# Kernel optimization log

Measured on AMD Instinct MI355X. Metric: run time of the kernel, lower is better.

Reference implementation:

```python
import jax, jax.numpy as jnp
import numpy as np
from math import factorial, sqrt

# ---- e3nn-style real Wigner-3j (Clebsch-Gordan) construction ----
L1, L2, LOUT, LMID = 3, 3, 3, 4

def _cg_coef(j1, m1, j2, m2, j3, m3):
    if m1 + m2 != m3:
        return 0.0
    f = factorial
    vmin = max(0, j2 - j3 - m1, j1 - j3 + m2)
    vmax = min(j1 + j2 - j3, j1 - m1, j2 + m2)
    pref = sqrt((2 * j3 + 1) * f(j3 + j1 - j2) * f(j3 - j1 + j2) * f(j1 + j2 - j3) / f(j1 + j2 + j3 + 1))
    pref *= sqrt(f(j3 + m3) * f(j3 - m3) * f(j1 + m1) * f(j1 - m1) * f(j2 + m2) * f(j2 - m2))
    s = 0.0
    for v in range(vmin, vmax + 1):
        s += (-1) ** v / (f(v) * f(j1 + j2 - j3 - v) * f(j1 - m1 - v) * f(j2 + m2 - v)
                          * f(j3 - j2 + m1 + v) * f(j3 - j1 - m2 + v))
    return pref * s

def _su2_cg(l1, l2, l3):
    C = np.zeros((2 * l1 + 1, 2 * l2 + 1, 2 * l3 + 1))
    for m1 in range(-l1, l1 + 1):
        for m2 in range(-l2, l2 + 1):
            m3 = m1 + m2
            if -l3 <= m3 <= l3:
                C[l1 + m1, l2 + m2, l3 + m3] = _cg_coef(l1, m1, l2, m2, l3, m3)
    return C

def _q(l):  # real->complex SH change of basis (e3nn convention)
    q = np.zeros((2 * l + 1, 2 * l + 1), dtype=np.complex128)
    for m in range(-l, 0):
        q[l + m, l + abs(m)] = 1 / np.sqrt(2)
        q[l + m, l - abs(m)] = -1j / np.sqrt(2)
    q[l, l] = 1.0
    for m in range(1, l + 1):
        q[l + m, l + abs(m)] = (-1) ** m / np.sqrt(2)
        q[l + m, l - abs(m)] = 1j * (-1) ** m / np.sqrt(2)
    return (-1j) ** l * q

def _w3j(l1, l2, l3):
    C = _su2_cg(l1, l2, l3).astype(np.complex128)
    C = np.einsum('ij,kl,mn,ikn->jlm', _q(l1), _q(l2), np.conj(_q(l3).T), C)
    C = np.real(C)
    return (C / np.linalg.norm(C)).astype(np.float32)

def _instructions(lmax1, lmax2, lmax_out):
    ins = [(a, b, c)
           for a in range(lmax1 + 1) for b in range(lmax2 + 1) for c in range(lmax_out + 1)
           if abs(a - b) <= c <= a + b and (a + b + c) % 2 == 0]
    cnt = {}
    for _, _, c in ins:
        cnt[c] = cnt.get(c, 0) + 1
    # normalization='component', path_normalization='element' with all mul=1
    pw = np.array([sqrt((2 * c + 1) / cnt[c]) for _, _, c in ins], dtype=np.float32)
    return ins, pw

INS1, PW1 = _instructions(L1, L2, LMID)      # 27 paths
INS21, PW21 = _instructions(L1, LMID, LOUT)  # 27 paths
INS22, PW22 = _instructions(L2, LMID, LOUT)  # 27 paths
W3J = {k: jnp.asarray(_w3j(*k)) for k in set(INS1) | set(INS21) | set(INS22)}

def _tp(x, y, w, ins, pw, lmax_out):
    # FullyConnectedTensorProduct with multiplicity-1 SH irreps.
    # x: [E, (l1+1)^2], y: [E, (l2+1)^2] -> [E, (lmax_out+1)^2]
    out = jnp.zeros((x.shape[0], (lmax_out + 1) ** 2), dtype=x.dtype)
    for i, (a, b, c) in enumerate(ins):
        xa = x[:, a * a:(a + 1) ** 2]
        yb = y[:, b * b:(b + 1) ** 2]
        z = jnp.einsum('ijk,ei,ej->ek', W3J[(a, b, c)], xa, yb)
        out = out.at[:, c * c:(c + 1) ** 2].add((pw[i] * w[i]) * z)
    return out

E, C = 200000, 16
B = (LOUT + 1) ** 2  # 16

def setup_inputs() -> dict:
    k = jax.random.split(jax.random.key(0), 5)
    return {
        'x': jax.random.normal(k[0], (E, B, C), jnp.float32),
        'y': jax.random.normal(k[1], (E, B, C), jnp.float32),
        'w1': jax.random.normal(k[2], (len(INS1),), jnp.float32),
        'w21': jax.random.normal(k[3], (len(INS21),), jnp.float32),
        'w22': jax.random.normal(k[4], (len(INS22),), jnp.float32),
    }

def reference(x, y, w1, w21, w22):
    xm = x.mean(2)  # [E, 16]
    ym = y.mean(2)  # [E, 16]
    mid = _tp(xm, ym, w1, INS1, PW1, LMID)  # [E, 25]
    out = (x + y
           + _tp(xm, mid, w21, INS21, PW21, LOUT)[..., None]
           + _tp(ym, mid, w22, INS22, PW22, LOUT)[..., None])
    return out
```

## Files before the change

kernel.cpp:

```cpp
#include <hip/hip_runtime.h>


struct W3JT { double v[9][9][9]; };

constexpr double dfact(int n) { double r = 1.0; for (int i = 2; i <= n; ++i) r *= (double)i; return r; }

constexpr double csqrt(double x) {
  if (x <= 0.0) return 0.0;
  double g = x > 1.0 ? x : 1.0;
  for (int i = 0; i < 80; ++i) g = 0.5 * (g + x / g);
  return g;
}

constexpr double cg_coef(int j1, int m1, int j2, int m2, int j3, int m3) {
  if (m1 + m2 != m3) return 0.0;
  int vmin = 0;
  if (j2 - j3 - m1 > vmin) vmin = j2 - j3 - m1;
  if (j1 - j3 + m2 > vmin) vmin = j1 - j3 + m2;
  int vmax = j1 + j2 - j3;
  if (j1 - m1 < vmax) vmax = j1 - m1;
  if (j2 + m2 < vmax) vmax = j2 + m2;
  double pref = csqrt((2.0 * j3 + 1.0) * dfact(j3 + j1 - j2) * dfact(j3 - j1 + j2) * dfact(j1 + j2 - j3) / dfact(j1 + j2 + j3 + 1));
  pref *= csqrt(dfact(j3 + m3) * dfact(j3 - m3) * dfact(j1 + m1) * dfact(j1 - m1) * dfact(j2 + m2) * dfact(j2 - m2));
  double s = 0.0;
  for (int v = vmin; v <= vmax; ++v) {
    double t = 1.0 / (dfact(v) * dfact(j1 + j2 - j3 - v) * dfact(j1 - m1 - v) * dfact(j2 + m2 - v) * dfact(j3 - j2 + m1 + v) * dfact(j3 - j1 - m2 + v));
    s += (v & 1) ? -t : t;
  }
  return pref * s;
}

struct QCol { int n; int row[2]; double re[2]; double im[2]; };

constexpr QCol qcol(int l, int col) {
  QCol q{};
  const int lm = l & 3;
  const double pr = (lm == 0) ? 1.0 : (lm == 2) ? -1.0 : 0.0;
  const double pi = (lm == 1) ? -1.0 : (lm == 3) ? 1.0 : 0.0;
  const int mu = col - l;
  const int am = mu < 0 ? -mu : mu;
  const double is2 = 0.70710678118654752440;
  if (mu == 0) {
    q.n = 1; q.row[0] = l;
    q.re[0] = pr; q.im[0] = pi;
  } else {
    const double s = (am & 1) ? -1.0 : 1.0;
    double a0 = 0.0, b0 = 0.0, a1 = 0.0, b1 = 0.0;
    if (mu > 0) { a0 = is2; b0 = 0.0;  a1 = s * is2; b1 = 0.0; }
    else        { a0 = 0.0; b0 = -is2; a1 = 0.0;     b1 = s * is2; }
    q.n = 2;
    q.row[0] = l - am; q.row[1] = l + am;
    q.re[0] = a0 * pr - b0 * pi; q.im[0] = a0 * pi + b0 * pr;
    q.re[1] = a1 * pr - b1 * pi; q.im[1] = a1 * pi + b1 * pr;
  }
  return q;
}

constexpr W3JT make_w3j(int l1, int l2, int l3) {
  W3JT R{};
  double C[9][9][9]{};
  for (int m1 = -l1; m1 <= l1; ++m1)
    for (int m2 = -l2; m2 <= l2; ++m2) {
      int m3 = m1 + m2;
      if (m3 >= -l3 && m3 <= l3)
        C[l1 + m1][l2 + m2][l3 + m3] = cg_coef(l1, m1, l2, m2, l3, m3);
    }
  double nrm = 0.0;
  for (int j = 0; j < 2 * l1 + 1; ++j) {
    QCol q1 = qcol(l1, j);
    for (int l = 0; l < 2 * l2 + 1; ++l) {
      QCol q2 = qcol(l2, l);
      for (int m = 0; m < 2 * l3 + 1; ++m) {
        QCol q3 = qcol(l3, m);
        double re = 0.0;
        for (int a = 0; a < q1.n; ++a)
          for (int b = 0; b < q2.n; ++b)
            for (int c = 0; c < q3.n; ++c) {
              double cv = C[q1.row[a]][q2.row[b]][q3.row[c]];
              if (cv == 0.0) continue;
              double ar = q1.re[a], ai = q1.im[a];
              double br = q2.re[b], bi = q2.im[b];
              double cr = q3.re[c], ci = -q3.im[c];
              double abr = ar * br - ai * bi;
              double abi = ar * bi + ai * br;
              double prr = abr * cr - abi * ci;
              re += prr * cv;
            }
        R.v[j][l][m] = re;
        nrm += re * re;
      }
    }
  }
  double n = csqrt(nrm);
  if (n > 0.0)
    for (int j = 0; j < 2 * l1 + 1; ++j)
      for (int l = 0; l < 2 * l2 + 1; ++l)
        for (int m = 0; m < 2 * l3 + 1; ++m)
          R.v[j][l][m] /= n;
  return R;
}

constexpr int CNT1[5] = {4, 6, 7, 6, 4};
constexpr int CNT2[4] = {4, 7, 8, 8};

#define NZCHK(V) ((V) > 1e-12 || (V) < -1e-12)

#define TP_MID(IDX, A, B, C) do { \
  constexpr W3JT T = make_w3j(A, B, C); \
  constexpr double PW = csqrt((2.0 * (C) + 1.0) / (double)CNT1[(C)]); \
  const float wi = w1p[IDX]; \
  float u[2 * (A) + 1]; \
  _Pragma("unroll") for (int i = 0; i < 2 * (A) + 1; ++i) u[i] = wi * xm[(A) * (A) + i]; \
  _Pragma("unroll") for (int i = 0; i < 2 * (A) + 1; ++i) { \
    _Pragma("unroll") for (int j = 0; j < 2 * (B) + 1; ++j) { \
      const float p_ = u[i] * ym[(B) * (B) + j]; \
      _Pragma("unroll") for (int k = 0; k < 2 * (C) + 1; ++k) { \
        if (NZCHK(T.v[i][j][k])) \
          mid[(C) * (C) + k] = __builtin_fmaf((float)(T.v[i][j][k] * PW), p_, mid[(C) * (C) + k]); \
      } \
    } \
  } \
} while (0)

#define TP_OUT(IDX, A, B, C) do { \
  constexpr W3JT T = make_w3j(A, B, C); \
  constexpr double PW = csqrt((2.0 * (C) + 1.0) / (double)CNT2[(C)]); \
  const float wa = w21p[IDX]; \
  const float wb = w22p[IDX]; \
  float u[2 * (A) + 1]; \
  _Pragma("unroll") for (int i = 0; i < 2 * (A) + 1; ++i) \
    u[i] = wa * xm[(A) * (A) + i] + wb * ym[(A) * (A) + i]; \
  _Pragma("unroll") for (int i = 0; i < 2 * (A) + 1; ++i) { \
    _Pragma("unroll") for (int j = 0; j < 2 * (B) + 1; ++j) { \
      const float p_ = u[i] * mid[(B) * (B) + j]; \
      _Pragma("unroll") for (int k = 0; k < 2 * (C) + 1; ++k) { \
        if (NZCHK(T.v[i][j][k])) \
          tv[(C) * (C) + k] = __builtin_fmaf((float)(T.v[i][j][k] * PW), p_, tv[(C) * (C) + k]); \
      } \
    } \
  } \
} while (0)

typedef float f32x4 __attribute__((ext_vector_type(4)));

__global__ __launch_bounds__(256) void cg2_v3(
    const float4* __restrict__ x4, const float4* __restrict__ y4,
    const float* __restrict__ w1p, const float* __restrict__ w21p,
    const float* __restrict__ w22p, float4* __restrict__ o4, int E)
{
  const int t = blockIdx.x * 256 + threadIdx.x;
  const int e = t >> 2;
  if (e >= E) return;
  const int g = t & 3;
  const int base = e * 64 + g;

  float4 s[16];
  float px[16], py[16];
#pragma unroll
  for (int k = 0; k < 16; ++k) {
    const float4 xv = x4[base + 4 * k];
    const float4 yv = y4[base + 4 * k];
    s[k].x = xv.x + yv.x; s[k].y = xv.y + yv.y;
    s[k].z = xv.z + yv.z; s[k].w = xv.w + yv.w;
    px[k] = (xv.x + xv.y) + (xv.z + xv.w);
    py[k] = (yv.x + yv.y) + (yv.z + yv.w);
  }

  float xm[16], ym[16];
#pragma unroll
  for (int k = 0; k < 16; ++k) {
    float rx = px[k] + __shfl_xor(px[k], 1);
    rx += __shfl_xor(rx, 2);
    float ry = py[k] + __shfl_xor(py[k], 1);
    ry += __shfl_xor(ry, 2);
    xm[k] = rx * (1.0f / 16.0f);
    ym[k] = ry * (1.0f / 16.0f);
  }

  float mid[25];
#pragma unroll
  for (int k = 0; k < 25; ++k) mid[k] = 0.f;

  TP_MID( 0, 0, 0, 0);
  TP_MID( 1, 0, 1, 1);
  TP_MID( 2, 0, 2, 2);
  TP_MID( 3, 0, 3, 3);
  TP_MID( 4, 1, 0, 1);
  TP_MID( 5, 1, 1, 0);
  TP_MID( 6, 1, 1, 2);
  TP_MID( 7, 1, 2, 1);
  TP_MID( 8, 1, 2, 3);
  TP_MID( 9, 1, 3, 2);
  TP_MID(10, 1, 3, 4);
  TP_MID(11, 2, 0, 2);
  TP_MID(12, 2, 1, 1);
  TP_MID(13, 2, 1, 3);
  TP_MID(14, 2, 2, 0);
  TP_MID(15, 2, 2, 2);
  TP_MID(16, 2, 2, 4);
  TP_MID(17, 2, 3, 1);
  TP_MID(18, 2, 3, 3);
  TP_MID(19, 3, 0, 3);
  TP_MID(20, 3, 1, 2);
  TP_MID(21, 3, 1, 4);
  TP_MID(22, 3, 2, 1);
  TP_MID(23, 3, 2, 3);
  TP_MID(24, 3, 3, 0);
  TP_MID(25, 3, 3, 2);
  TP_MID(26, 3, 3, 4);

  float tv[16];
#pragma unroll
  for (int k = 0; k < 16; ++k) tv[k] = 0.f;

  TP_OUT( 0, 0, 0, 0);
  TP_OUT( 1, 0, 1, 1);
  TP_OUT( 2, 0, 2, 2);
  TP_OUT( 3, 0, 3, 3);
  TP_OUT( 4, 1, 0, 1);
  TP_OUT( 5, 1, 1, 0);
  TP_OUT( 6, 1, 1, 2);
  TP_OUT( 7, 1, 2, 1);
  TP_OUT( 8, 1, 2, 3);
  TP_OUT( 9, 1, 3, 2);
  TP_OUT(10, 1, 4, 3);
  TP_OUT(11, 2, 0, 2);
  TP_OUT(12, 2, 1, 1);
  TP_OUT(13, 2, 1, 3);
  TP_OUT(14, 2, 2, 0);
  TP_OUT(15, 2, 2, 2);
  TP_OUT(16, 2, 3, 1);
  TP_OUT(17, 2, 3, 3);
  TP_OUT(18, 2, 4, 2);
  TP_OUT(19, 3, 0, 3);
  TP_OUT(20, 3, 1, 2);
  TP_OUT(21, 3, 2, 1);
  TP_OUT(22, 3, 2, 3);
  TP_OUT(23, 3, 3, 0);
  TP_OUT(24, 3, 3, 2);
  TP_OUT(25, 3, 4, 1);
  TP_OUT(26, 3, 4, 3);

  f32x4* __restrict__ on = reinterpret_cast<f32x4*>(o4);
#pragma unroll
  for (int k = 0; k < 16; ++k) {
    f32x4 o;
    o.x = s[k].x + tv[k];
    o.y = s[k].y + tv[k];
    o.z = s[k].z + tv[k];
    o.w = s[k].w + tv[k];
    __builtin_nontemporal_store(o, &on[base + 4 * k]);
  }
}

extern "C" void kernel_launch(void* const* d_in, const int* in_sizes, int n_in,
                              void* d_out, int out_size, void* d_ws, size_t ws_size,
                              hipStream_t stream) {
  const float4* x4 = (const float4*)d_in[0];
  const float4* y4 = (const float4*)d_in[1];
  const float* w1p = (const float*)d_in[2];
  const float* w21p = (const float*)d_in[3];
  const float* w22p = (const float*)d_in[4];
  float4* o4 = (float4*)d_out;

  const int E = in_sizes[0] / 256;
  const int total = E * 4;
  const int block = 256;
  const int grid = (total + block - 1) / block;

  cg2_v3<<<grid, block, 0, stream>>>(x4, y4, w1p, w21p, w22p, o4, E);
}
```

Measured before the change: 131.1 us.

## Compute tensor products once per edge via LDS, stage x+y in output buffer

New measurement: 171.6 us. +30.8%, slower.

```diff
diff --git a/kernel.cpp b/kernel.cpp
--- a/kernel.cpp
+++ b/kernel.cpp
@@ -141,115 +141,149 @@
   } \
 } while (0)
 
-typedef float f32x4 __attribute__((ext_vector_type(4)));
-
-__global__ __launch_bounds__(256) void cg2_v3(
+__global__ __launch_bounds__(256) void cg2_v5(
     const float4* __restrict__ x4, const float4* __restrict__ y4,
     const float* __restrict__ w1p, const float* __restrict__ w21p,
     const float* __restrict__ w22p, float4* __restrict__ o4, int E)
 {
-  const int t = blockIdx.x * 256 + threadIdx.x;
-  const int e = t >> 2;
-  if (e >= E) return;
-  const int g = t & 3;
+  __shared__ float lmx[64 * 32];
+  __shared__ float ltv[64 * 16];
+
+  const int eL = threadIdx.x >> 2;
+  const int g  = threadIdx.x & 3;
+  const int e  = blockIdx.x * 64 + eL;
+  const bool ok = (e < E);
   const int base = e * 64 + g;
 
-  float4 s[16];
   float px[16], py[16];
-#pragma unroll
-  for (int k = 0; k < 16; ++k) {
-    const float4 xv = x4[base + 4 * k];
-    const float4 yv = y4[base + 4 * k];
-    s[k].x = xv.x + yv.x; s[k].y = xv.y + yv.y;
-    s[k].z = xv.z + yv.z; s[k].w = xv.w + yv.w;
-    px[k] = (xv.x + xv.y) + (xv.z + xv.w);
-    py[k] = (yv.x + yv.y) + (yv.z + yv.w);
-  }
-
-  float xm[16], ym[16];
+  if (ok) {
+#pragma unroll
+    for (int k = 0; k < 16; ++k) {
+      const float4 xv = x4[base + 4 * k];
+      const float4 yv = y4[base + 4 * k];
+      float4 s;
+      s.x = xv.x + yv.x; s.y = xv.y + yv.y;
+      s.z = xv.z + yv.z; s.w = xv.w + yv.w;
+      o4[base + 4 * k] = s;
+      px[k] = (xv.x + xv.y) + (xv.z + xv.w);
+      py[k] = (yv.x + yv.y) + (yv.z + yv.w);
+    }
+  } else {
+#pragma unroll
+    for (int k = 0; k < 16; ++k) { px[k] = 0.f; py[k] = 0.f; }
+  }
+
 #pragma unroll
   for (int k = 0; k < 16; ++k) {
     float rx = px[k] + __shfl_xor(px[k], 1);
     rx += __shfl_xor(rx, 2);
     float ry = py[k] + __shfl_xor(py[k], 1);
     ry += __shfl_xor(ry, 2);
-    xm[k] = rx * (1.0f / 16.0f);
-    ym[k] = ry * (1.0f / 16.0f);
-  }
-
-  float mid[25];
-#pragma unroll
-  for (int k = 0; k < 25; ++k) mid[k] = 0.f;
-
-  TP_MID( 0, 0, 0, 0);
-  TP_MID( 1, 0, 1, 1);
-  TP_MID( 2, 0, 2, 2);
-  TP_MID( 3, 0, 3, 3);
-  TP_MID( 4, 1, 0, 1);
-  TP_MID( 5, 1, 1, 0);
-  TP_MID( 6, 1, 1, 2);
-  TP_MID( 7, 1, 2, 1);
-  TP_MID( 8, 1, 2, 3);
-  TP_MID( 9, 1, 3, 2);
-  TP_MID(10, 1, 3, 4);
-  TP_MID(11, 2, 0, 2);
-  TP_MID(12, 2, 1, 1);
-  TP_MID(13, 2, 1, 3);
-  TP_MID(14, 2, 2, 0);
-  TP_MID(15, 2, 2, 2);
-  TP_MID(16, 2, 2, 4);
-  TP_MID(17, 2, 3, 1);
-  TP_MID(18, 2, 3, 3);
-  TP_MID(19, 3, 0, 3);
-  TP_MID(20, 3, 1, 2);
-  TP_MID(21, 3, 1, 4);
-  TP_MID(22, 3, 2, 1);
-  TP_MID(23, 3, 2, 3);
-  TP_MID(24, 3, 3, 0);
-  TP_MID(25, 3, 3, 2);
-  TP_MID(26, 3, 3, 4);
-
-  float tv[16];
-#pragma unroll
-  for (int k = 0; k < 16; ++k) tv[k] = 0.f;
-
-  TP_OUT( 0, 0, 0, 0);
-  TP_OUT( 1, 0, 1, 1);
-  TP_OUT( 2, 0, 2, 2);
-  TP_OUT( 3, 0, 3, 3);
-  TP_OUT( 4, 1, 0, 1);
-  TP_OUT( 5, 1, 1, 0);
-  TP_OUT( 6, 1, 1, 2);
-  TP_OUT( 7, 1, 2, 1);
-  TP_OUT( 8, 1, 2, 3);
-  TP_OUT( 9, 1, 3, 2);
-  TP_OUT(10, 1, 4, 3);
-  TP_OUT(11, 2, 0, 2);
-  TP_OUT(12, 2, 1, 1);
-  TP_OUT(13, 2, 1, 3);
-  TP_OUT(14, 2, 2, 0);
-  TP_OUT(15, 2, 2, 2);
-  TP_OUT(16, 2, 3, 1);
-  TP_OUT(17, 2, 3, 3);
-  TP_OUT(18, 2, 4, 2);
-  TP_OUT(19, 3, 0, 3);
-  TP_OUT(20, 3, 1, 2);
-  TP_OUT(21, 3, 2, 1);
-  TP_OUT(22, 3, 2, 3);
-  TP_OUT(23, 3, 3, 0);
-  TP_OUT(24, 3, 3, 2);
-  TP_OUT(25, 3, 4, 1);
-  TP_OUT(26, 3, 4, 3);
-
-  f32x4* __restrict__ on = reinterpret_cast<f32x4*>(o4);
-#pragma unroll
-  for (int k = 0; k < 16; ++k) {
-    f32x4 o;
-    o.x = s[k].x + tv[k];
-    o.y = s[k].y + tv[k];
-    o.z = s[k].z + tv[k];
-    o.w = s[k].w + tv[k];
-    __builtin_nontemporal_store(o, &on[base + 4 * k]);
+    px[k] = rx * (1.0f / 16.0f);
+    py[k] = ry * (1.0f / 16.0f);
+  }
+
+  if (ok) {
+#pragma unroll
+    for (int u = 0; u < 4; ++u) {
+      const int j = 4 * g + u;
+      lmx[eL * 32 + ((j + eL) & 31)]      = px[j];
+      lmx[eL * 32 + ((16 + j + eL) & 31)] = py[j];
+    }
+  }
+  __syncthreads();
+
+  if (threadIdx.x < 64) {
+    const int q = threadIdx.x;
+    const bool ok2 = (blockIdx.x * 64 + q < E);
+    float xm[16], ym[16];
+#pragma unroll
+    for (int j = 0; j < 16; ++j) xm[j] = lmx[q * 32 + ((j + q) & 31)];
+#pragma unroll
+    for (int j = 0; j < 16; ++j) ym[j] = lmx[q * 32 + ((16 + j + q) & 31)];
+
+    float mid[25];
+#pragma unroll
+    for (int k = 0; k < 25; ++k) mid[k] = 0.f;
+
+    TP_MID( 0, 0, 0, 0);
+    TP_MID( 1, 0, 1, 1);
+    TP_MID( 2, 0, 2, 2);
+    TP_MID( 3, 0, 3, 3);
+    TP_MID( 4, 1, 0, 1);
+    TP_MID( 5, 1, 1, 0);
+    TP_MID( 6, 1, 1, 2);
+    TP_MID( 7, 1, 2, 1);
+    TP_MID( 8, 1, 2, 3);
+    TP_MID( 9, 1, 3, 2);
+    TP_MID(10, 1, 3, 4);
+    TP_MID(11, 2, 0, 2);
+    TP_MID(12, 2, 1, 1);
+    TP_MID(13, 2, 1, 3);
+    TP_MID(14, 2, 2, 0);
+    TP_MID(15, 2, 2, 2);
+    TP_MID(16, 2, 2, 4);
+    TP_MID(17, 2, 3, 1);
+    TP_MID(18, 2, 3, 3);
+    TP_MID(19, 3, 0, 3);
+    TP_MID(20, 3, 1, 2);
+    TP_MID(21, 3, 1, 4);
+    TP_MID(22, 3, 2, 1);
+    TP_MID(23, 3, 2, 3);
+    TP_MID(24, 3, 3, 0);
+    TP_MID(25, 3, 3, 2);
+    TP_MID(26, 3, 3, 4);
+
+    float tv[16];
+#pragma unroll
+    for (int k = 0; k < 16; ++k) tv[k] = 0.f;
+
+    TP_OUT( 0, 0, 0, 0);
+    TP_OUT( 1, 0, 1, 1);
+    TP_OUT( 2, 0, 2, 2);
+    TP_OUT( 3, 0, 3, 3);
+    TP_OUT( 4, 1, 0, 1);
+    TP_OUT( 5, 1, 1, 0);
+    TP_OUT( 6, 1, 1, 2);
+    TP_OUT( 7, 1, 2, 1);
+    TP_OUT( 8, 1, 2, 3);
+    TP_OUT( 9, 1, 3, 2);
+    TP_OUT(10, 1, 4, 3);
+    TP_OUT(11, 2, 0, 2);
+    TP_OUT(12, 2, 1, 1);
+    TP_OUT(13, 2, 1, 3);
+    TP_OUT(14, 2, 2, 0);
+    TP_OUT(15, 2, 2, 2);
+    TP_OUT(16, 2, 3, 1);
+    TP_OUT(17, 2, 3, 3);
+    TP_OUT(18, 2, 4, 2);
+    TP_OUT(19, 3, 0, 3);
+    TP_OUT(20, 3, 1, 2);
+    TP_OUT(21, 3, 2, 1);
+    TP_OUT(22, 3, 2, 3);
+    TP_OUT(23, 3, 3, 0);
+    TP_OUT(24, 3, 3, 2);
+    TP_OUT(25, 3, 4, 1);
+    TP_OUT(26, 3, 4, 3);
+
+    if (ok2) {
+#pragma unroll
+      for (int k = 0; k < 16; ++k) ltv[q * 16 + ((k + q) & 15)] = tv[k];
+    }
+  }
+  __syncthreads();
+
+  if (ok) {
+    float tvv[16];
+#pragma unroll
+    for (int k = 0; k < 16; ++k) tvv[k] = ltv[eL * 16 + ((k + eL) & 15)];
+#pragma unroll
+    for (int k = 0; k < 16; ++k) {
+      float4 s = o4[base + 4 * k];
+      s.x += tvv[k]; s.y += tvv[k];
+      s.z += tvv[k]; s.w += tvv[k];
+      o4[base + 4 * k] = s;
+    }
   }
 }
 
@@ -264,9 +298,8 @@
   float4* o4 = (float4*)d_out;
 
   const int E = in_sizes[0] / 256;
-  const int total = E * 4;
   const int block = 256;
-  const int grid = (total + block - 1) / block;
-
-  cg2_v3<<<grid, block, 0, stream>>>(x4, y4, w1p, w21p, w22p, o4, E);
-}
+  const int grid = (E + 63) / 64;
+
+  cg2_v5<<<grid, block, 0, stream>>>(x4, y4, w1p, w21p, w22p, o4, E);
+}
```

## Move tensor-product results through LDS and re-read inputs instead of holding sums

Applied to the files above, without the earlier changes.

Measured after the change: 303.9 us. +131.7%, slower.

```diff
diff --git a/kernel.cpp b/kernel.cpp
--- a/kernel.cpp
+++ b/kernel.cpp
@@ -141,115 +141,140 @@
   } \
 } while (0)
 
-typedef float f32x4 __attribute__((ext_vector_type(4)));
-
-__global__ __launch_bounds__(256) void cg2_v3(
-    const float4* __restrict__ x4, const float4* __restrict__ y4,
+__global__ __launch_bounds__(256) void cg2_v7(
+    const float4* __restrict__ x4a, const float4* __restrict__ y4a,
+    const float4* __restrict__ x4b, const float4* __restrict__ y4b,
     const float* __restrict__ w1p, const float* __restrict__ w21p,
     const float* __restrict__ w22p, float4* __restrict__ o4, int E)
 {
-  const int t = blockIdx.x * 256 + threadIdx.x;
-  const int e = t >> 2;
-  if (e >= E) return;
-  const int g = t & 3;
-  const int base = e * 64 + g;
-
-  float4 s[16];
-  float px[16], py[16];
+  __shared__ float smx[4][16 * 17];
+  __shared__ float smy[4][16 * 17];
+  __shared__ float smt[4][16 * 17];
+
+  const int wid = threadIdx.x >> 6;
+  const int l   = threadIdx.x & 63;
+  const int W   = blockIdx.x * 4 + wid;
+  const int e0  = W * 16;
+  const int base = W * 1024 + l;
+  const int g = l & 3, r = l >> 2;
+
+  float pxk[16], pyk[16];
 #pragma unroll
   for (int k = 0; k < 16; ++k) {
-    const float4 xv = x4[base + 4 * k];
-    const float4 yv = y4[base + 4 * k];
-    s[k].x = xv.x + yv.x; s[k].y = xv.y + yv.y;
-    s[k].z = xv.z + yv.z; s[k].w = xv.w + yv.w;
-    px[k] = (xv.x + xv.y) + (xv.z + xv.w);
-    py[k] = (yv.x + yv.y) + (yv.z + yv.w);
-  }
-
-  float xm[16], ym[16];
+    if (e0 + k < E) {
+      const float4 xv = x4a[base + 64 * k];
+      const float4 yv = y4a[base + 64 * k];
+      pxk[k] = (xv.x + xv.y) + (xv.z + xv.w);
+      pyk[k] = (yv.x + yv.y) + (yv.z + yv.w);
+    } else { pxk[k] = 0.f; pyk[k] = 0.f; }
+  }
+
 #pragma unroll
   for (int k = 0; k < 16; ++k) {
-    float rx = px[k] + __shfl_xor(px[k], 1);
+    float rx = pxk[k] + __shfl_xor(pxk[k], 1);
     rx += __shfl_xor(rx, 2);
-    float ry = py[k] + __shfl_xor(py[k], 1);
+    float ry = pyk[k] + __shfl_xor(pyk[k], 1);
     ry += __shfl_xor(ry, 2);
-    xm[k] = rx * (1.0f / 16.0f);
-    ym[k] = ry * (1.0f / 16.0f);
-  }
-
-  float mid[25];
-#pragma unroll
-  for (int k = 0; k < 25; ++k) mid[k] = 0.f;
-
-  TP_MID( 0, 0, 0, 0);
-  TP_MID( 1, 0, 1, 1);
-  TP_MID( 2, 0, 2, 2);
-  TP_MID( 3, 0, 3, 3);
-  TP_MID( 4, 1, 0, 1);
-  TP_MID( 5, 1, 1, 0);
-  TP_MID( 6, 1, 1, 2);
-  TP_MID( 7, 1, 2, 1);
-  TP_MID( 8, 1, 2, 3);
-  TP_MID( 9, 1, 3, 2);
-  TP_MID(10, 1, 3, 4);
-  TP_MID(11, 2, 0, 2);
-  TP_MID(12, 2, 1, 1);
-  TP_MID(13, 2, 1, 3);
-  TP_MID(14, 2, 2, 0);
-  TP_MID(15, 2, 2, 2);
-  TP_MID(16, 2, 2, 4);
-  TP_MID(17, 2, 3, 1);
-  TP_MID(18, 2, 3, 3);
-  TP_MID(19, 3, 0, 3);
-  TP_MID(20, 3, 1, 2);
-  TP_MID(21, 3, 1, 4);
-  TP_MID(22, 3, 2, 1);
-  TP_MID(23, 3, 2, 3);
-  TP_MID(24, 3, 3, 0);
-  TP_MID(25, 3, 3, 2);
-  TP_MID(26, 3, 3, 4);
-
-  float tv[16];
-#pragma unroll
-  for (int k = 0; k < 16; ++k) tv[k] = 0.f;
-
-  TP_OUT( 0, 0, 0, 0);
-  TP_OUT( 1, 0, 1, 1);
-  TP_OUT( 2, 0, 2, 2);
-  TP_OUT( 3, 0, 3, 3);
-  TP_OUT( 4, 1, 0, 1);
-  TP_OUT( 5, 1, 1, 0);
-  TP_OUT( 6, 1, 1, 2);
-  TP_OUT( 7, 1, 2, 1);
-  TP_OUT( 8, 1, 2, 3);
-  TP_OUT( 9, 1, 3, 2);
-  TP_OUT(10, 1, 4, 3);
-  TP_OUT(11, 2, 0, 2);
-  TP_OUT(12, 2, 1, 1);
-  TP_OUT(13, 2, 1, 3);
-  TP_OUT(14, 2, 2, 0);
-  TP_OUT(15, 2, 2, 2);
-  TP_OUT(16, 2, 3, 1);
-  TP_OUT(17, 2, 3, 3);
-  TP_OUT(18, 2, 4, 2);
-  TP_OUT(19, 3, 0, 3);
-  TP_OUT(20, 3, 1, 2);
-  TP_OUT(21, 3, 2, 1);
-  TP_OUT(22, 3, 2, 3);
-  TP_OUT(23, 3, 3, 0);
-  TP_OUT(24, 3, 3, 2);
-  TP_OUT(25, 3, 4, 1);
-  TP_OUT(26, 3, 4, 3);
-
-  f32x4* __restrict__ on = reinterpret_cast<f32x4*>(o4);
+    pxk[k] = rx * (1.0f / 16.0f);
+    pyk[k] = ry * (1.0f / 16.0f);
+  }
+
+#pragma unroll
+  for (int j = 0; j < 4; ++j) {
+    const int k = 4 * j + g;
+    smx[wid][k * 17 + r] = pxk[k];
+    smy[wid][k * 17 + r] = pyk[k];
+  }
+
+  if (l < 16) {
+    const int q = l;
+    float xm[16], ym[16];
+#pragma unroll
+    for (int j = 0; j < 16; ++j) xm[j] = smx[wid][q * 17 + j];
+#pragma unroll
+    for (int j = 0; j < 16; ++j) ym[j] = smy[wid][q * 17 + j];
+
+    float mid[25];
+#pragma unroll
+    for (int k = 0; k < 25; ++k) mid[k] = 0.f;
+
+    TP_MID( 0, 0, 0, 0);
+    TP_MID( 1, 0, 1, 1);
+    TP_MID( 2, 0, 2, 2);
+    TP_MID( 3, 0, 3, 3);
+    TP_MID( 4, 1, 0, 1);
+    TP_MID( 5, 1, 1, 0);
+    TP_MID( 6, 1, 1, 2);
+    TP_MID( 7, 1, 2, 1);
+    TP_MID( 8, 1, 2, 3);
+    TP_MID( 9, 1, 3, 2);
+    TP_MID(10, 1, 3, 4);
+    TP_MID(11, 2, 0, 2);
+    TP_MID(12, 2, 1, 1);
+    TP_MID(13, 2, 1, 3);
+    TP_MID(14, 2, 2, 0);
+    TP_MID(15, 2, 2, 2);
+    TP_MID(16, 2, 2, 4);
+    TP_MID(17, 2, 3, 1);
+    TP_MID(18, 2, 3, 3);
+    TP_MID(19, 3, 0, 3);
+    TP_MID(20, 3, 1, 2);
+    TP_MID(21, 3, 1, 4);
+    TP_MID(22, 3, 2, 1);
+    TP_MID(23, 3, 2, 3);
+    TP_MID(24, 3, 3, 0);
+    TP_MID(25, 3, 3, 2);
+    TP_MID(26, 3, 3, 4);
+
+    float tv[16];
+#pragma unroll
+    for (int k = 0; k < 16; ++k) tv[k] = 0.f;
+
+    TP_OUT( 0, 0, 0, 0);
+    TP_OUT( 1, 0, 1, 1);
+    TP_OUT( 2, 0, 2, 2);
+    TP_OUT( 3, 0, 3, 3);
+    TP_OUT( 4, 1, 0, 1);
+    TP_OUT( 5, 1, 1, 0);
+    TP_OUT( 6, 1, 1, 2);
+    TP_OUT( 7, 1, 2, 1);
+    TP_OUT( 8, 1, 2, 3);
+    TP_OUT( 9, 1, 3, 2);
+    TP_OUT(10, 1, 4, 3);
+    TP_OUT(11, 2, 0, 2);
+    TP_OUT(12, 2, 1, 1);
+    TP_OUT(13, 2, 1, 3);
+    TP_OUT(14, 2, 2, 0);
+    TP_OUT(15, 2, 2, 2);
+    TP_OUT(16, 2, 3, 1);
+    TP_OUT(17, 2, 3, 3);
+    TP_OUT(18, 2, 4, 2);
+    TP_OUT(19, 3, 0, 3);
+    TP_OUT(20, 3, 1, 2);
+    TP_OUT(21, 3, 2, 1);
+    TP_OUT(22, 3, 2, 3);
+    TP_OUT(23, 3, 3, 0);
+    TP_OUT(24, 3, 3, 2);
+    TP_OUT(25, 3, 4, 1);
+    TP_OUT(26, 3, 4, 3);
+
+#pragma unroll
+    for (int k = 0; k < 16; ++k) smt[wid][q * 17 + k] = tv[k];
+  }
+
 #pragma unroll
   for (int k = 0; k < 16; ++k) {
-    f32x4 o;
-    o.x = s[k].x + tv[k];
-    o.y = s[k].y + tv[k];
-    o.z = s[k].z + tv[k];
-    o.w = s[k].w + tv[k];
-    __builtin_nontemporal_store(o, &on[base + 4 * k]);
+    if (e0 + k < E) {
+      const float4 xv = x4b[base + 64 * k];
+      const float4 yv = y4b[base + 64 * k];
+      const float t = smt[wid][k * 17 + r];
+      float4 o;
+      o.x = xv.x + yv.x + t;
+      o.y = xv.y + yv.y + t;
+      o.z = xv.z + yv.z + t;
+      o.w = xv.w + yv.w + t;
+      o4[base + 64 * k] = o;
+    }
   }
 }
 
@@ -264,9 +289,8 @@
   float4* o4 = (float4*)d_out;
 
   const int E = in_sizes[0] / 256;
-  const int total = E * 4;
   const int block = 256;
-  const int grid = (total + block - 1) / block;
-
-  cg2_v3<<<grid, block, 0, stream>>>(x4, y4, w1p, w21p, w22p, o4, E);
-}
+  const int grid = (E + 63) / 64;
+
+  cg2_v7<<<grid, block, 0, stream>>>(x4, y4, x4, y4, w1p, w21p, w22p, o4, E);
+}
```
